# Kernel tuning notes

Measured on AMD Instinct MI355X. Metric: run time of the kernel, lower is better.

Reference implementation:

```python
import jax, jax.numpy as jnp
import numpy as np

D = 512          # d_model
DS = 32          # d_state
EXPAND = 2
HEADDIM = 64
R = 4            # mimo_rank
DIN = EXPAND * D             # 1024 inner dim
H = DIN // HEADDIM           # 16 heads
DFF = ((int(D * 8 / 3) + 7) // 8) * 8  # 1368 SwiGLU hidden
CHUNK = max(1, 64 // R)      # 16
BATCH, SEQ = 4, 512


def setup_inputs() -> dict:
    key = jax.random.key(0)
    ks = jax.random.split(key, 12)
    def w(k, shape, fan):
        return jax.random.normal(k, shape, jnp.float32) / np.float32(np.sqrt(fan))
    return {
        "x": jax.random.normal(ks[0], (BATCH, SEQ, D), jnp.float32),
        "mask": jnp.ones((BATCH, SEQ), jnp.float32),
        "norm1_w": jnp.ones((D,), jnp.float32),
        "norm2_w": jnp.ones((D,), jnp.float32),
        "Wz": w(ks[1], (D, DIN), D),
        "Wx": w(ks[2], (D, DIN), D),
        "Wb": w(ks[3], (D, H * R * DS), D),
        "Wc": w(ks[4], (D, H * R * DS), D),
        "Wdt": w(ks[5], (D, H), D),
        "dt_bias": jnp.zeros((H,), jnp.float32),
        "A_log": jnp.log(jnp.arange(1, H + 1, dtype=jnp.float32)),
        "D_skip": jnp.ones((H,), jnp.float32),
        "Wout": w(ks[6], (DIN, D), DIN),
        "w1": w(ks[7], (D, DFF), D),
        "w2": w(ks[8], (DFF, D), DFF),
        "w3": w(ks[9], (D, DFF), D),
    }


def rmsnorm(x, wgt, eps=1e-6):
    rms = jnp.sqrt(jnp.mean(x * x, axis=-1, keepdims=True) + eps)
    return x / rms * wgt


def ssm_mixer(x, Wz, Wx, Wb, Wc, Wdt, dt_bias, A_log, D_skip, Wout):
    # x: [B, S, D] (already masked)
    B, S, _ = x.shape
    pad = (CHUNK - S % CHUNK) % CHUNK
    if pad > 0:
        x = jnp.pad(x, ((0, 0), (0, pad), (0, 0)))
    Sp = x.shape[1]
    z = x @ Wz                                        # [B,Sp,DIN] gate
    u = (x @ Wx).reshape(B, Sp, H, HEADDIM)           # [B,Sp,H,P]
    Bm = (x @ Wb).reshape(B, Sp, H, R, DS)            # [B,Sp,H,R,N]
    Cm = (x @ Wc).reshape(B, Sp, H, R, DS)
    dt = jax.nn.softplus(x @ Wdt + dt_bias)           # [B,Sp,H]
    a = jnp.exp(dt * (-jnp.exp(A_log)))               # per-step decay [B,Sp,H]
    ud = u * dt[..., None]                            # discretized input

    def step(h, inp):
        a_t, B_t, C_t, ud_t = inp                     # [B,H], [B,H,R,N], [B,H,R,N], [B,H,P]
        h = a_t[:, :, None, None, None] * h + jnp.einsum('bhrn,bhp->bhrnp', B_t, ud_t)
        y = jnp.einsum('bhrn,bhrnp->bhp', C_t, h)
        return h, y

    h0 = jnp.zeros((B, H, R, DS, HEADDIM), x.dtype)
    xs = (a.swapaxes(0, 1), Bm.swapaxes(0, 1), Cm.swapaxes(0, 1), ud.swapaxes(0, 1))
    _, ys = jax.lax.scan(step, h0, xs)                # ys: [Sp,B,H,P]
    y = ys.swapaxes(0, 1) + u * D_skip[None, None, :, None]
    y = y.reshape(B, Sp, DIN) * jax.nn.silu(z)
    y = y @ Wout                                      # [B,Sp,D]
    return y[:, :S]


def reference(x, mask, norm1_w, norm2_w, Wz, Wx, Wb, Wc, Wdt, dt_bias,
              A_log, D_skip, Wout, w1, w2, w3):
    m = mask[..., None]
    xn = rmsnorm(x, norm1_w) * m
    y = ssm_mixer(xn, Wz, Wx, Wb, Wc, Wdt, dt_bias, A_log, D_skip, Wout) * m
    x = x + y
    xn2 = rmsnorm(x, norm2_w)
    x = x + (jax.nn.silu(xn2 @ w1) * (xn2 @ w3)) @ w2
    return x * m
```

## Files before the change

kernel.cpp:

```cpp
#include <hip/hip_runtime.h>
#include <hip/hip_bf16.h>
#include <math.h>

#define Bn 4
#define Sn 512
#define Dn 512
#define DINn 1024
#define Hn 16
#define Pn 64
#define RNn 128
#define DFFn 1368
#define KP2 1408
#define BSn (Bn*Sn)
#define CH 64
#define NCH (Sn/CH)
#define PSTR 6144
#define FSTR 2736
#define FPAD 2816
#define NSCAN (Bn*NCH*Hn)

typedef __attribute__((ext_vector_type(8))) short short8;
typedef __attribute__((ext_vector_type(4))) float f32x4;
typedef __attribute__((ext_vector_type(4))) short short4v;

static __device__ __forceinline__ float bf2f(__hip_bfloat16 v){return __bfloat162float(v);}
static __device__ __forceinline__ __hip_bfloat16 f2bf(float v){return __float2bfloat16(v);}
static __device__ __forceinline__ short f2bfs(float v){ __hip_bfloat16 b=f2bf(v); short s; __builtin_memcpy(&s,&b,2); return s; }
static __device__ __forceinline__ float bfs2f(short s){ __hip_bfloat16 b; __builtin_memcpy(&b,&s,2); return bf2f(b); }

typedef const __attribute__((address_space(1))) unsigned int* gas1_u32p;
typedef __attribute__((address_space(3))) unsigned int* gas3_u32p;
static __device__ __forceinline__ void gl_lds16(const void* g, void* l) {
  __builtin_amdgcn_global_load_lds((gas1_u32p)g, (gas3_u32p)l, 16, 0, 0);
}

struct T8 {
  const float* src[8];
  __hip_bfloat16* dst[8];
  int Rr[8], Cc[8], RrPad[8], CcPad[8], gw[8];
  int start[9];
};

static __device__ __forceinline__ void transpose_tile(const T8& d, int bid, int t,
                                                      float (*tile)[65]) {
  int i = 0;
#pragma unroll
  for (int k = 1; k < 8; ++k) if (bid >= d.start[k]) i = k;
  int rel = bid - d.start[i];
  int gx = rel % d.gw[i], gy = rel / d.gw[i];
  const float* in = d.src[i];
  __hip_bfloat16* out = d.dst[i];
  int Rr = d.Rr[i], Cc = d.Cc[i], RrPad = d.RrPad[i], CcPad = d.CcPad[i];
  int tx = t & 15, ty = t >> 4;
#pragma unroll
  for (int i4 = 0; i4 < 4; ++i4) {
    int r = gy * 64 + ty + i4 * 16;
    int c0 = gx * 64 + tx * 4;
    f32x4 v = (f32x4){0.f, 0.f, 0.f, 0.f};
    if (r < Rr && c0 + 3 < Cc) v = *(const f32x4*)(in + (size_t)r * Cc + c0);
    tile[ty + i4 * 16][tx * 4 + 0] = v[0];
    tile[ty + i4 * 16][tx * 4 + 1] = v[1];
    tile[ty + i4 * 16][tx * 4 + 2] = v[2];
    tile[ty + i4 * 16][tx * 4 + 3] = v[3];
  }
  __syncthreads();
#pragma unroll
  for (int i4 = 0; i4 < 4; ++i4) {
    int r2 = gx * 64 + ty + i4 * 16;
    int c2 = gy * 64 + tx * 4;
    if (r2 < CcPad && c2 + 3 < RrPad) {
      int k = ty + i4 * 16;
      short4v o;
      o.x = f2bfs(tile[tx * 4 + 0][k]);
      o.y = f2bfs(tile[tx * 4 + 1][k]);
      o.z = f2bfs(tile[tx * 4 + 2][k]);
      o.w = f2bfs(tile[tx * 4 + 3][k]);
      *(short4v*)((short*)out + (size_t)r2 * RrPad + c2) = o;
    }
  }
}

__global__ __launch_bounds__(256) void prep_kernel(
    T8 d, const float* __restrict__ x, const float* __restrict__ w,
    const float* __restrict__ mask, const float* __restrict__ Wdt,
    const float* __restrict__ dtb, const float* __restrict__ Alog,
    __hip_bfloat16* __restrict__ outb, float* __restrict__ dt,
    float* __restrict__ la, int tstart) {
  __shared__ float tile[64][65];
  __shared__ float xs[Dn];
  __shared__ float red[4];
  int bid = blockIdx.x, t = threadIdx.x;
  if (bid < tstart) {
    transpose_tile(d, bid, t, tile);
  } else {
    int row = bid - tstart;
    const float* xr = x + (size_t)row * Dn;
    float v0 = xr[t], v1 = xr[t + 256];
    float ss = v0 * v0 + v1 * v1;
#pragma unroll
    for (int o = 32; o > 0; o >>= 1) ss += __shfl_down(ss, o);
    if ((t & 63) == 0) red[t >> 6] = ss;
    __syncthreads();
    float tot = red[0] + red[1] + red[2] + red[3];
    float sc = rsqrtf(tot * (1.f / Dn) + 1e-6f) * mask[row];
    float o0 = v0 * sc * w[t], o1v = v1 * sc * w[t + 256];
    outb[(size_t)row * Dn + t] = f2bf(o0);
    outb[(size_t)row * Dn + t + 256] = f2bf(o1v);
    xs[t] = o0;
    xs[t + 256] = o1v;
    __syncthreads();
    int h = t >> 4, j = t & 15;
    float s = 0.f;
#pragma unroll
    for (int kk = 0; kk < 32; ++kk) {
      int k = j + kk * 16;
      s = fmaf(xs[k], Wdt[k * Hn + h], s);
    }
#pragma unroll
    for (int o = 8; o > 0; o >>= 1) s += __shfl_down(s, o, 16);
    if (j == 0) {
      float v = s + dtb[h];
      float sp = (v > 20.f) ? v : log1pf(expf(v));
      float Ah = expf(Alog[h]);
      dt[(size_t)row * Hn + h] = sp;
      la[(size_t)row * Hn + h] = -Ah * sp;
    }
  }
}

__global__ void rmsnorm2_kernel(const float* __restrict__ x,
                                const float* __restrict__ w,
                                __hip_bfloat16* __restrict__ out) {
  int row = blockIdx.x, t = threadIdx.x;
  const float* xr = x + (size_t)row * Dn;
  float v0 = xr[t], v1 = xr[t + 256];
  float ss = v0 * v0 + v1 * v1;
#pragma unroll
  for (int o = 32; o > 0; o >>= 1) ss += __shfl_down(ss, o);
  __shared__ float red[4];
  if ((t & 63) == 0) red[t >> 6] = ss;
  __syncthreads();
  float tot = red[0] + red[1] + red[2] + red[3];
  float sc = rsqrtf(tot * (1.f / Dn) + 1e-6f);
  out[(size_t)row * Dn + t] = f2bf(v0 * sc * w[t]);
  out[(size_t)row * Dn + t + 256] = f2bf(v1 * sc * w[t + 256]);
}

__global__ __launch_bounds__(256) void gemm_kernel(
    const __hip_bfloat16* __restrict__ A, const __hip_bfloat16* __restrict__ BT,
    __hip_bfloat16* __restrict__ C, int M, int N, int K) {
  __shared__ short As[2][4096];
  __shared__ short Bs[2][4096];
  int m0 = blockIdx.x * 128, n0 = blockIdx.y * 128;
  int t = threadIdx.x;
  int lane = t & 63, wv = t >> 6;
  int wm = (wv & 1) * 64, wn = (wv >> 1) * 64;
  f32x4 acc[4][4];
#pragma unroll
  for (int i = 0; i < 4; ++i)
#pragma unroll
    for (int j = 0; j < 4; ++j) acc[i][j] = (f32x4){0.f, 0.f, 0.f, 0.f};
  const short* Ag = (const short*)A;
  const short* Bg = (const short*)BT;
  int r0 = t >> 2, p = t & 3;
  int q0 = (p - (r0 >> 1)) & 3;
  int r1 = r0 + 64;
  int q1 = (p - (r1 >> 1)) & 3;
  const short* Asrc0 = Ag + (size_t)(m0 + r0) * K + 8 * q0;
  const short* Asrc1 = Ag + (size_t)(m0 + r1) * K + 8 * q1;
  const short* Bsrc0 = Bg + (size_t)(n0 + r0) * K + 8 * q0;
  const short* Bsrc1 = Bg + (size_t)(n0 + r1) * K + 8 * q1;
  int fr = lane & 15, fq = lane >> 4;
  int kTiles = K >> 5;
  auto stage = [&](int buf, int k0) {
    gl_lds16(Asrc0 + k0, &As[buf][wv * 512]);
    gl_lds16(Asrc1 + k0, &As[buf][2048 + wv * 512]);
    gl_lds16(Bsrc0 + k0, &Bs[buf][wv * 512]);
    gl_lds16(Bsrc1 + k0, &Bs[buf][2048 + wv * 512]);
  };
  auto domfma = [&](int buf) {
    short8 af[4], bfr[4];
#pragma unroll
    for (int i = 0; i < 4; ++i) {
      int rr = wm + i * 16 + fr;
      af[i] = *(const short8*)&As[buf][rr * 32 + (((rr >> 1) + fq) & 3) * 8];
    }
#pragma unroll
    for (int i = 0; i < 4; ++i) {
      int rr = wn + i * 16 + fr;
      bfr[i] = *(const short8*)&Bs[buf][rr * 32 + (((rr >> 1) + fq) & 3) * 8];
    }
#pragma unroll
    for (int mi = 0; mi < 4; ++mi)
#pragma unroll
      for (int ni = 0; ni < 4; ++ni)
        acc[mi][ni] = __builtin_amdgcn_mfma_f32_16x16x32_bf16(af[mi], bfr[ni], acc[mi][ni], 0, 0, 0);
  };
  stage(0, 0);
  for (int kt = 0; kt < kTiles; ++kt) {
    int buf = kt & 1;
    __syncthreads();
    if (kt + 1 < kTiles) stage(buf ^ 1, (kt + 1) << 5);
    domfma(buf);
  }
  int fq4 = (lane >> 4) * 4;
#pragma unroll
  for (int mi = 0; mi < 4; ++mi)
#pragma unroll
    for (int ni = 0; ni < 4; ++ni) {
      int col = n0 + wn + ni * 16 + fr;
      if (col < N) {
        int rowb = m0 + wm + mi * 16 + fq4;
#pragma unroll
        for (int r = 0; r < 4; ++r)
          C[(size_t)(rowb + r) * N + col] = f2bf(acc[mi][ni][r]);
      }
    }
}

template <int MODE>
__global__ __launch_bounds__(256) void gemm64_ep_kernel(
    const __hip_bfloat16* __restrict__ A, const __hip_bfloat16* __restrict__ BT,
    const float* __restrict__ aux, const float* __restrict__ mask,
    float* __restrict__ out, int M, int N, int K) {
  __shared__ short As[2][64][72];
  __shared__ short Bs[2][64][72];
  int m0 = blockIdx.x * 64, n0 = blockIdx.y * 64;
  int t = threadIdx.x;
  int lane = t & 63, wv = t >> 6;
  int wm = (wv & 1) * 32, wn = (wv >> 1) * 32;
  f32x4 acc[2][2];
#pragma unroll
  for (int i = 0; i < 2; ++i)
#pragma unroll
    for (int j = 0; j < 2; ++j) acc[i][j] = (f32x4){0.f, 0.f, 0.f, 0.f};
  const short* Ag = (const short*)A;
  const short* Bg = (const short*)BT;
  int sr = t >> 2;
  int sc = (t & 3) * 16;
  const short* Ap = Ag + (size_t)(m0 + sr) * K + sc;
  const short* Bp = Bg + (size_t)(n0 + sr) * K + sc;
  int fr = lane & 15, fq = (lane >> 4) * 8;
  int kTiles = K >> 6;
  short8 a0A = 0, a1A = 0, b0A = 0, b1A = 0;
  short8 a0B = 0, a1B = 0, b0B = 0, b1B = 0;
  auto loadA = [&](int k0) {
    a0A = *(const short8*)(Ap + k0);
    a1A = *(const short8*)(Ap + k0 + 8);
    b0A = *(const short8*)(Bp + k0);
    b1A = *(const short8*)(Bp + k0 + 8);
  };
  auto loadB = [&](int k0) {
    a0B = *(const short8*)(Ap + k0);
    a1B = *(const short8*)(Ap + k0 + 8);
    b0B = *(const short8*)(Bp + k0);
    b1B = *(const short8*)(Bp + k0 + 8);
  };
  auto storeA = [&](int buf) {
    *(short8*)&As[buf][sr][sc] = a0A;
    *(short8*)&As[buf][sr][sc + 8] = a1A;
    *(short8*)&Bs[buf][sr][sc] = b0A;
    *(short8*)&Bs[buf][sr][sc + 8] = b1A;
  };
  auto storeB = [&](int buf) {
    *(short8*)&As[buf][sr][sc] = a0B;
    *(short8*)&As[buf][sr][sc + 8] = a1B;
    *(short8*)&Bs[buf][sr][sc] = b0B;
    *(short8*)&Bs[buf][sr][sc + 8] = b1B;
  };
  auto mfma = [&](int buf) {
#pragma unroll
    for (int kk = 0; kk < 2; ++kk) {
      short8 af[2], bfr[2];
#pragma unroll
      for (int i = 0; i < 2; ++i) af[i] = *(const short8*)&As[buf][wm + i * 16 + fr][kk * 32 + fq];
#pragma unroll
      for (int i = 0; i < 2; ++i) bfr[i] = *(const short8*)&Bs[buf][wn + i * 16 + fr][kk * 32 + fq];
#pragma unroll
      for (int mi = 0; mi < 2; ++mi)
#pragma unroll
        for (int ni = 0; ni < 2; ++ni)
          acc[mi][ni] = __builtin_amdgcn_mfma_f32_16x16x32_bf16(af[mi], bfr[ni], acc[mi][ni], 0, 0, 0);
    }
  };
  loadA(0);
  storeA(0);
  loadA(64);
  __syncthreads();
  for (int kt = 0; kt < kTiles; kt += 2) {
    storeA(1);
    if (kt + 2 < kTiles) loadB((kt + 2) << 6);
    mfma(0);
    __syncthreads();
    if (kt + 2 < kTiles) storeB(0);
    if (kt + 3 < kTiles) loadA((kt + 3) << 6);
    mfma(1);
    __syncthreads();
  }
  int fq4 = (lane >> 4) * 4;
#pragma unroll
  for (int mi = 0; mi < 2; ++mi)
#pragma unroll
    for (int ni = 0; ni < 2; ++ni) {
      int col = n0 + wn + ni * 16 + fr;
#pragma unroll
      for (int r = 0; r < 4; ++r) {
        int row = m0 + wm + mi * 16 + fq4 + r;
        float m = mask[row];
        size_t a = (size_t)row * N + col;
        float v = acc[mi][ni][r];
        if (MODE == 1) out[a] = aux[a] + v * m;
        else           out[a] = (aux[a] + v) * m;
      }
    }
}

__global__ __launch_bounds__(256) void gemm64g_kernel(
    const __hip_bfloat16* __restrict__ A, const __hip_bfloat16* __restrict__ BT,
    __hip_bfloat16* __restrict__ G, int M, int K) {
  __shared__ short As[2][64][72];
  __shared__ short B1s[2][64][72];
  __shared__ short B3s[2][64][72];
  int m0 = blockIdx.x * 64, n0 = blockIdx.y * 64;
  int t = threadIdx.x;
  int lane = t & 63, wv = t >> 6;
  int wm = (wv & 1) * 32, wn = (wv >> 1) * 32;
  f32x4 acc1[2][2], acc3[2][2];
#pragma unroll
  for (int i = 0; i < 2; ++i)
#pragma unroll
    for (int j = 0; j < 2; ++j) {
      acc1[i][j] = (f32x4){0.f, 0.f, 0.f, 0.f};
      acc3[i][j] = (f32x4){0.f, 0.f, 0.f, 0.f};
    }
  const short* Ag = (const short*)A;
  const short* Bg = (const short*)BT;
  int sr = t >> 2;
  int sc = (t & 3) * 16;
  const short* Ap  = Ag + (size_t)(m0 + sr) * K + sc;
  const short* B1p = Bg + (size_t)(n0 + sr) * K + sc;
  const short* B3p = Bg + (size_t)(DFFn + n0 + sr) * K + sc;
  int fr = lane & 15, fq = (lane >> 4) * 8;
  int kTiles = K >> 6;
  short8 a0A = 0, a1A = 0, c0A = 0, c1A = 0, d0A = 0, d1A = 0;
  short8 a0B = 0, a1B = 0, c0B = 0, c1B = 0, d0B = 0, d1B = 0;
  auto loadA = [&](int k0) {
    a0A = *(const short8*)(Ap + k0);
    a1A = *(const short8*)(Ap + k0 + 8);
    c0A = *(const short8*)(B1p + k0);
    c1A = *(const short8*)(B1p + k0 + 8);
    d0A = *(const short8*)(B3p + k0);
    d1A = *(const short8*)(B3p + k0 + 8);
  };
  auto loadB = [&](int k0) {
    a0B = *(const short8*)(Ap + k0);
    a1B = *(const short8*)(Ap + k0 + 8);
    c0B = *(const short8*)(B1p + k0);
    c1B = *(const short8*)(B1p + k0 + 8);
    d0B = *(const short8*)(B3p + k0);
    d1B = *(const short8*)(B3p + k0 + 8);
  };
  auto storeA = [&](int buf) {
    *(short8*)&As[buf][sr][sc] = a0A;
    *(short8*)&As[buf][sr][sc + 8] = a1A;
    *(short8*)&B1s[buf][sr][sc] = c0A;
    *(short8*)&B1s[buf][sr][sc + 8] = c1A;
    *(short8*)&B3s[buf][sr][sc] = d0A;
    *(short8*)&B3s[buf][sr][sc + 8] = d1A;
  };
  auto storeB = [&](int buf) {
    *(short8*)&As[buf][sr][sc] = a0B;
    *(short8*)&As[buf][sr][sc + 8] = a1B;
    *(short8*)&B1s[buf][sr][sc] = c0B;
    *(short8*)&B1s[buf][sr][sc + 8] = c1B;
    *(short8*)&B3s[buf][sr][sc] = d0B;
    *(short8*)&B3s[buf][sr][sc + 8] = d1B;
  };
  auto mfma = [&](int buf) {
#pragma unroll
    for (int kk = 0; kk < 2; ++kk) {
      short8 af[2], b1f[2], b3f[2];
#pragma unroll
      for (int i = 0; i < 2; ++i) af[i]  = *(const short8*)&As[buf][wm + i * 16 + fr][kk * 32 + fq];
#pragma unroll
      for (int i = 0; i < 2; ++i) b1f[i] = *(const short8*)&B1s[buf][wn + i * 16 + fr][kk * 32 + fq];
#pragma unroll
      for (int i = 0; i < 2; ++i) b3f[i] = *(const short8*)&B3s[buf][wn + i * 16 + fr][kk * 32 + fq];
#pragma unroll
      for (int mi = 0; mi < 2; ++mi)
#pragma unroll
        for (int ni = 0; ni < 2; ++ni) {
          acc1[mi][ni] = __builtin_amdgcn_mfma_f32_16x16x32_bf16(af[mi], b1f[ni], acc1[mi][ni], 0, 0, 0);
          acc3[mi][ni] = __builtin_amdgcn_mfma_f32_16x16x32_bf16(af[mi], b3f[ni], acc3[mi][ni], 0, 0, 0);
        }
    }
  };
  loadA(0);
  storeA(0);
  loadA(64);
  __syncthreads();
  for (int kt = 0; kt < kTiles; kt += 2) {
    storeA(1);
    if (kt + 2 < kTiles) loadB((kt + 2) << 6);
    mfma(0);
    __syncthreads();
    if (kt + 2 < kTiles) storeB(0);
    if (kt + 3 < kTiles) loadA((kt + 3) << 6);
    mfma(1);
    __syncthreads();
  }
  int fq4 = (lane >> 4) * 4;
#pragma unroll
  for (int mi = 0; mi < 2; ++mi)
#pragma unroll
    for (int ni = 0; ni < 2; ++ni) {
      int col = n0 + wn + ni * 16 + fr;
      bool valid = col < DFFn;
#pragma unroll
      for (int r = 0; r < 4; ++r) {
        int row = m0 + wm + mi * 16 + fq4 + r;
        float h1v = acc1[mi][ni][r];
        float sil = h1v / (1.f + __expf(-h1v));
        float g = sil * acc3[mi][ni][r];
        G[(size_t)row * KP2 + col] = valid ? f2bf(g) : f2bf(0.f);
      }
    }
}

__global__ __launch_bounds__(256) void chunk_intra_kernel(
    T8 d, int nscan, const __hip_bfloat16* __restrict__ P, const float* __restrict__ dt,
    const float* __restrict__ la, __hip_bfloat16* __restrict__ ysb,
    __hip_bfloat16* __restrict__ Sbuf, float* __restrict__ ecL, float* __restrict__ ec) {
  __shared__ __align__(16) char smem[55040];
  int bid0 = blockIdx.x;
  int t = threadIdx.x;
  if (bid0 >= nscan) {
    transpose_tile(d, bid0 - nscan, t, (float(*)[65])smem);
    return;
  }
  int id = bid0;
  int h = id & 15, c = (id >> 4) & 7, b = id >> 7;
  int lane = t & 63, wv = t >> 6;
  short* sCB = (short*)smem;
  short* sB  = (short*)(smem + 18432);
  short* sUD = (short*)(smem + 35840);
  short* sG  = (short*)(smem + 45056);
  float* scum = (float*)(smem + 54272);
  float* sws  = scum + 64;
  float* sdt  = sws + 64;
  int row0 = b * Sn + c * CH;
  const short* Pb = (const short*)P;
#pragma unroll
  for (int i = 0; i < 4; ++i) {
    int idx = t + i * 256;
    int r = idx >> 4, kk = (idx & 15) * 8;
    *(short8*)&sCB[r * 136 + kk] = *(const short8*)(Pb + (size_t)(row0 + r) * PSTR + 4096 + h * 128 + kk);
    *(short8*)&sB [r * 136 + kk] = *(const short8*)(Pb + (size_t)(row0 + r) * PSTR + 2048 + h * 128 + kk);
  }
  if (t < 64) { sdt[t] = dt[(size_t)(row0 + t) * Hn + h]; scum[t] = la[(size_t)(row0 + t) * Hn + h]; }
  __syncthreads();
  if (wv == 0) {
    float v = scum[lane];
#pragma unroll
    for (int o = 1; o < 64; o <<= 1) { float n = __shfl_up(v, o); if (lane >= o) v += n; }
    scum[lane] = v;
    float c63 = __shfl(v, 63);
    sws[lane] = __expf(c63 - v);
    ec[((size_t)((b * NCH + c) * Hn + h)) * 64 + lane] = __expf(v);
    if (lane == 0) ecL[(b * NCH + c) * Hn + h] = __expf(c63);
  }
#pragma unroll
  for (int i = 0; i < 2; ++i) {
    int idx = t + i * 256;
    int s = idx >> 3, pc = (idx & 7) * 8;
    short8 uv = *(const short8*)(Pb + (size_t)(row0 + s) * PSTR + 1024 + h * 64 + pc);
    float dv = sdt[s];
#pragma unroll
    for (int j = 0; j < 8; ++j) sUD[(pc + j) * 72 + s] = f2bfs(bfs2f(uv[j]) * dv);
  }
  __syncthreads();
  int fr = lane & 15, fq = (lane >> 4) * 8, q4 = (lane >> 4) * 4;
  {
    short8 af[4];
#pragma unroll
    for (int k = 0; k < 4; ++k) af[k] = *(short8*)&sCB[(16 * wv + fr) * 136 + k * 32 + fq];
#pragma unroll
    for (int j = 0; j < 4; ++j) {
      f32x4 acc = (f32x4){0.f, 0.f, 0.f, 0.f};
#pragma unroll
      for (int k = 0; k < 4; ++k) {
        short8 bf = *(short8*)&sB[(16 * j + fr) * 136 + k * 32 + fq];
        acc = __builtin_amdgcn_mfma_f32_16x16x32_bf16(af[k], bf, acc, 0, 0, 0);
      }
      int ss = 16 * j + fr;
      float cs = scum[ss];
#pragma unroll
      for (int r = 0; r < 4; ++r) {
        int tt = 16 * wv + q4 + r;
        float w = (ss <= tt) ? __expf(scum[tt] - cs) : 0.f;
        sG[tt * 72 + ss] = f2bfs(acc[r] * w);
      }
    }
  }
  __syncthreads();
#pragma unroll
  for (int i = 0; i < 32; ++i) {
    int idx = t + i * 256;
    int rn = idx >> 6, s = idx & 63;
    sCB[rn * 72 + s] = f2bfs(bfs2f(sB[s * 136 + rn]) * sws[s]);
  }
  __syncthreads();
  {
    short8 ag[2];
#pragma unroll
    for (int k = 0; k < 2; ++k) ag[k] = *(short8*)&sG[(16 * wv + fr) * 72 + k * 32 + fq];
#pragma unroll
    for (int j = 0; j < 4; ++j) {
      f32x4 acc = (f32x4){0.f, 0.f, 0.f, 0.f};
#pragma unroll
      for (int k = 0; k < 2; ++k) {
        short8 bf = *(short8*)&sUD[(16 * j + fr) * 72 + k * 32 + fq];
        acc = __builtin_amdgcn_mfma_f32_16x16x32_bf16(ag[k], bf, acc, 0, 0, 0);
      }
#pragma unroll
      for (int r = 0; r < 4; ++r)
        ysb[(size_t)(row0 + 16 * wv + q4 + r) * DINn + h * 64 + 16 * j + fr] = f2bf(acc[r]);
    }
  }
#pragma unroll
  for (int mt0 = 0; mt0 < 2; ++mt0) {
    int mt = wv * 2 + mt0;
    short8 ab[2];
#pragma unroll
    for (int k = 0; k < 2; ++k) ab[k] = *(short8*)&sCB[(16 * mt + fr) * 72 + k * 32 + fq];
#pragma unroll
    for (int j = 0; j < 4; ++j) {
      f32x4 acc = (f32x4){0.f, 0.f, 0.f, 0.f};
#pragma unroll
      for (int k = 0; k < 2; ++k) {
        short8 bf = *(short8*)&sUD[(16 * j + fr) * 72 + k * 32 + fq];
        acc = __builtin_amdgcn_mfma_f32_16x16x32_bf16(ab[k], bf, acc, 0, 0, 0);
      }
#pragma unroll
      for (int r = 0; r < 4; ++r)
        ((short*)Sbuf)[((size_t)((b * NCH + c) * Hn + h) * RNn + 16 * mt + q4 + r) * 64 + 16 * j + fr] =
            f2bfs(acc[r]);
    }
  }
}

__global__ void chunk_state_kernel(const __hip_bfloat16* __restrict__ Sbuf,
                                   const float* __restrict__ ecL,
                                   __hip_bfloat16* __restrict__ Hp) {
  int bh = blockIdx.x >> 4;
  int j = ((blockIdx.x & 15) * 256 + threadIdx.x) * 2;
  int b = bh >> 4, h = bh & 15;
  const short* Sb = (const short*)Sbuf;
  short* Hs = (short*)Hp;
  float hp0 = 0.f, hp1 = 0.f;
#pragma unroll
  for (int c = 0; c < NCH; ++c) {
    size_t addr = ((size_t)((b * NCH + c) * Hn + h)) * 8192 + j;
    short2 sv = *(const short2*)(Sb + addr);
    *(short2*)(Hs + addr) = make_short2(f2bfs(hp0), f2bfs(hp1));
    float e = ecL[(b * NCH + c) * Hn + h];
    hp0 = e * hp0 + bfs2f(sv.x);
    hp1 = e * hp1 + bfs2f(sv.y);
  }
}

__global__ __launch_bounds__(256) void inter_gate_kernel(
    const __hip_bfloat16* __restrict__ P, const __hip_bfloat16* __restrict__ Hp,
    const float* __restrict__ ec, const __hip_bfloat16* __restrict__ ysb,
    const float* __restrict__ Dsk, __hip_bfloat16* __restrict__ y2b) {
  int id = blockIdx.x;
  int h = id & 15, c = (id >> 4) & 7, b = id >> 7;
  int t = threadIdx.x, lane = t & 63, wv = t >> 6;
  __shared__ __align__(16) short sC[64 * 136];
  __shared__ __align__(16) short sHt[64 * 136];
  __shared__ __align__(16) short sz[64 * 64];
  __shared__ __align__(16) short su[64 * 64];
  __shared__ float sec[64];
  int row0 = b * Sn + c * CH;
  const short* Pb = (const short*)P;
#pragma unroll
  for (int i = 0; i < 2; ++i) {
    int idx = t + i * 256;
    int r = idx >> 3, pc = (idx & 7) * 8;
    *(short8*)&sz[r * 64 + pc] = *(const short8*)(Pb + (size_t)(row0 + r) * PSTR + h * 64 + pc);
    *(short8*)&su[r * 64 + pc] = *(const short8*)(Pb + (size_t)(row0 + r) * PSTR + 1024 + h * 64 + pc);
  }
  if (c > 0) {
    const short* Hps = (const short*)Hp;
    size_t hbase = ((size_t)((b * NCH + c) * Hn + h)) * 8192;
#pragma unroll
    for (int i = 0; i < 4; ++i) {
      int idx = t + i * 256;
      int r = idx >> 4, kk = (idx & 15) * 8;
      *(short8*)&sC[r * 136 + kk] = *(const short8*)(Pb + (size_t)(row0 + r) * PSTR + 4096 + h * 128 + kk);
    }
#pragma unroll
    for (int i = 0; i < 32; ++i) {
      int idx = t + i * 256;
      int rn = idx >> 6, p = idx & 63;
      sHt[p * 136 + rn] = Hps[hbase + idx];
    }
    if (t < 64) sec[t] = ec[((size_t)((b * NCH + c) * Hn + h)) * 64 + t];
  }
  __syncthreads();
  int fr = lane & 15, fq = (lane >> 4) * 8, q4 = (lane >> 4) * 4;
  f32x4 acc[4];
#pragma unroll
  for (int j = 0; j < 4; ++j) acc[j] = (f32x4){0.f, 0.f, 0.f, 0.f};
  if (c > 0) {
    short8 af[4];
#pragma unroll
    for (int k = 0; k < 4; ++k) af[k] = *(short8*)&sC[(16 * wv + fr) * 136 + k * 32 + fq];
#pragma unroll
    for (int j = 0; j < 4; ++j)
#pragma unroll
      for (int k = 0; k < 4; ++k) {
        short8 bf = *(short8*)&sHt[(16 * j + fr) * 136 + k * 32 + fq];
        acc[j] = __builtin_amdgcn_mfma_f32_16x16x32_bf16(af[k], bf, acc[j], 0, 0, 0);
      }
  }
  float dsk = Dsk[h];
#pragma unroll
  for (int j = 0; j < 4; ++j) {
    int col = 16 * j + fr;
#pragma unroll
    for (int r = 0; r < 4; ++r) {
      int tt = 16 * wv + q4 + r;
      size_t a = (size_t)(row0 + tt) * DINn + h * 64 + col;
      float val = bf2f(ysb[a]);
      if (c > 0) val += sec[tt] * acc[j][r];
      float uu = bfs2f(su[tt * 64 + col]);
      float zz = bfs2f(sz[tt * 64 + col]);
      float sil = zz / (1.f + __expf(-zz));
      y2b[a] = f2bf((val + uu * dsk) * sil);
    }
  }
}

extern "C" void kernel_launch(void* const* d_in, const int* in_sizes, int n_in,
                              void* d_out, int out_size, void* d_ws, size_t ws_size,
                              hipStream_t stream) {
  const float* x    = (const float*)d_in[0];
  const float* mask = (const float*)d_in[1];
  const float* n1w  = (const float*)d_in[2];
  const float* n2w  = (const float*)d_in[3];
  const float* Wz   = (const float*)d_in[4];
  const float* Wx   = (const float*)d_in[5];
  const float* Wb   = (const float*)d_in[6];
  const float* Wc   = (const float*)d_in[7];
  const float* Wdt  = (const float*)d_in[8];
  const float* dtb  = (const float*)d_in[9];
  const float* Alog = (const float*)d_in[10];
  const float* Dsk  = (const float*)d_in[11];
  const float* Wout = (const float*)d_in[12];
  const float* w1   = (const float*)d_in[13];
  const float* w2   = (const float*)d_in[14];
  const float* w3   = (const float*)d_in[15];

  char* ws = (char*)d_ws;
  size_t off = 0;
  auto alloc = [&](size_t bytes) {
    char* p = ws + off;
    off += (bytes + 255) & ~(size_t)255;
    return p;
  };
  __hip_bfloat16* xnb = (__hip_bfloat16*)alloc((size_t)BSn * Dn * 2);
  __hip_bfloat16* P = (__hip_bfloat16*)alloc((size_t)BSn * PSTR * 2);
  float* dt  = (float*)alloc((size_t)BSn * Hn * 4);
  float* la  = (float*)alloc((size_t)BSn * Hn * 4);
  __hip_bfloat16* ysb = (__hip_bfloat16*)alloc((size_t)BSn * DINn * 2);
  float* ecL = (float*)alloc((size_t)Bn * NCH * Hn * 4);
  float* ec  = (float*)alloc((size_t)Bn * NCH * Hn * 64 * 4);
  __hip_bfloat16* WallT = (__hip_bfloat16*)alloc((size_t)PSTR * Dn * 2);
  __hip_bfloat16* WoutT = (__hip_bfloat16*)alloc((size_t)Dn * DINn * 2);
  __hip_bfloat16* w13T  = (__hip_bfloat16*)alloc((size_t)FPAD * Dn * 2);
  __hip_bfloat16* w2T   = (__hip_bfloat16*)alloc((size_t)Dn * KP2 * 2);
  char* arena = alloc(22000000);
  __hip_bfloat16* Sbuf = (__hip_bfloat16*)arena;
  __hip_bfloat16* Hp   = (__hip_bfloat16*)(arena + 8388608);
  __hip_bfloat16* y2b  = (__hip_bfloat16*)(arena + 16777216);
  float* xres          = (float*)arena;
  __hip_bfloat16* gatedb = (__hip_bfloat16*)(arena + 4194304);

  auto buildT8 = [](T8& td, int n) {
    int tot = 0;
    for (int i = 0; i < n; ++i) {
      td.gw[i] = (td.CcPad[i] + 63) / 64;
      int gh = (td.RrPad[i] + 63) / 64;
      td.start[i] = tot;
      tot += td.gw[i] * gh;
    }
    for (int i = n; i < 9; ++i) td.start[i] = tot;
    return tot;
  };
  T8 tdE;
  tdE.src[0] = Wz; tdE.dst[0] = WallT;                      tdE.Rr[0] = 512; tdE.Cc[0] = 1024; tdE.RrPad[0] = 512; tdE.CcPad[0] = 1024;
  tdE.src[1] = Wx; tdE.dst[1] = WallT + (size_t)1024 * 512; tdE.Rr[1] = 512; tdE.Cc[1] = 1024; tdE.RrPad[1] = 512; tdE.CcPad[1] = 1024;
  tdE.src[2] = Wb; tdE.dst[2] = WallT + (size_t)2048 * 512; tdE.Rr[2] = 512; tdE.Cc[2] = 2048; tdE.RrPad[2] = 512; tdE.CcPad[2] = 2048;
  tdE.src[3] = Wc; tdE.dst[3] = WallT + (size_t)4096 * 512; tdE.Rr[3] = 512; tdE.Cc[3] = 2048; tdE.RrPad[3] = 512; tdE.CcPad[3] = 2048;
  int totE = buildT8(tdE, 4);
  T8 tdL;
  tdL.src[0] = Wout; tdL.dst[0] = WoutT;                     tdL.Rr[0] = 1024; tdL.Cc[0] = 512;  tdL.RrPad[0] = 1024; tdL.CcPad[0] = 512;
  tdL.src[1] = w1;   tdL.dst[1] = w13T;                      tdL.Rr[1] = 512;  tdL.Cc[1] = 1368; tdL.RrPad[1] = 512;  tdL.CcPad[1] = 1368;
  tdL.src[2] = w3;   tdL.dst[2] = w13T + (size_t)1368 * 512; tdL.Rr[2] = 512;  tdL.Cc[2] = 1368; tdL.RrPad[2] = 512;  tdL.CcPad[2] = 1448;
  tdL.src[3] = w2;   tdL.dst[3] = w2T;                       tdL.Rr[3] = 1368; tdL.Cc[3] = 512;  tdL.RrPad[3] = KP2;  tdL.CcPad[3] = 512;
  int totL = buildT8(tdL, 4);

  prep_kernel<<<totE + BSn, 256, 0, stream>>>(tdE, x, n1w, mask, Wdt, dtb, Alog, xnb, dt, la, totE);
  gemm_kernel<<<dim3(16, 48), 256, 0, stream>>>(xnb, WallT, P, BSn, PSTR, Dn);
  chunk_intra_kernel<<<NSCAN + totL, 256, 0, stream>>>(tdL, NSCAN, P, dt, la, ysb, Sbuf, ecL, ec);
  chunk_state_kernel<<<Bn * Hn * 16, 256, 0, stream>>>(Sbuf, ecL, Hp);
  inter_gate_kernel<<<Bn * NCH * Hn, 256, 0, stream>>>(P, Hp, ec, ysb, Dsk, y2b);
  gemm64_ep_kernel<1><<<dim3(32, 8), 256, 0, stream>>>(y2b, WoutT, x, mask, xres, BSn, Dn, DINn);
  rmsnorm2_kernel<<<BSn, 256, 0, stream>>>(xres, n2w, xnb);
  gemm64g_kernel<<<dim3(32, KP2 / 64), 256, 0, stream>>>(xnb, w13T, gatedb, BSn, Dn);
  gemm64_ep_kernel<2><<<dim3(32, 8), 256, 0, stream>>>(gatedb, w2T, xres, mask, (float*)d_out, BSn, Dn, KP2);
}
```

Measured before the change: 210.3 us.

## Fuse inter-chunk state recurrence into gate kernel and RMSNorm2 into FFN GEMM

Removes the separate chunk_state kernel: each inter_gate block now rebuilds its incoming state by summing the earlier chunk states, weighted by products of chunk decays, read straight from Sbuf, whose layout is transposed to suit this. The second RMSNorm kernel goes away: the Wout GEMM epilogue atomically adds per-row sums of squares, and the FFN GEMM applies the normalisation while converting fp32 activations to bf16 on load. All weight transposes move into prep_kernel, which also zeroes the row-sum buffer. Together this saves two launches and the Hp round trip through memory. In exchange, later chunks repeat O(c) state reads, atomics are added, and the FFN A-operand is read as fp32.

```diff
diff --git a/kernel.cpp b/kernel.cpp
--- a/kernel.cpp
+++ b/kernel.cpp
@@ -15,7 +15,6 @@
 #define CH 64
 #define NCH (Sn/CH)
 #define PSTR 6144
-#define FSTR 2736
 #define FPAD 2816
 #define NSCAN (Bn*NCH*Hn)
 
@@ -85,14 +84,14 @@
     const float* __restrict__ mask, const float* __restrict__ Wdt,
     const float* __restrict__ dtb, const float* __restrict__ Alog,
     __hip_bfloat16* __restrict__ outb, float* __restrict__ dt,
-    float* __restrict__ la, int tstart) {
+    float* __restrict__ la, float* __restrict__ rs, int tstart) {
   __shared__ float tile[64][65];
   __shared__ float xs[Dn];
   __shared__ float red[4];
   int bid = blockIdx.x, t = threadIdx.x;
   if (bid < tstart) {
     transpose_tile(d, bid, t, tile);
-  } else {
+  } else if (bid - tstart < BSn) {
     int row = bid - tstart;
     const float* xr = x + (size_t)row * Dn;
     float v0 = xr[t], v1 = xr[t + 256];
@@ -125,25 +124,10 @@
       dt[(size_t)row * Hn + h] = sp;
       la[(size_t)row * Hn + h] = -Ah * sp;
     }
-  }
-}
-
-__global__ void rmsnorm2_kernel(const float* __restrict__ x,
-                                const float* __restrict__ w,
-                                __hip_bfloat16* __restrict__ out) {
-  int row = blockIdx.x, t = threadIdx.x;
-  const float* xr = x + (size_t)row * Dn;
-  float v0 = xr[t], v1 = xr[t + 256];
-  float ss = v0 * v0 + v1 * v1;
-#pragma unroll
-  for (int o = 32; o > 0; o >>= 1) ss += __shfl_down(ss, o);
-  __shared__ float red[4];
-  if ((t & 63) == 0) red[t >> 6] = ss;
-  __syncthreads();
-  float tot = red[0] + red[1] + red[2] + red[3];
-  float sc = rsqrtf(tot * (1.f / Dn) + 1e-6f);
-  out[(size_t)row * Dn + t] = f2bf(v0 * sc * w[t]);
-  out[(size_t)row * Dn + t + 256] = f2bf(v1 * sc * w[t + 256]);
+  } else {
+    *(f32x4*)&rs[t * 8]     = (f32x4){0.f, 0.f, 0.f, 0.f};
+    *(f32x4*)&rs[t * 8 + 4] = (f32x4){0.f, 0.f, 0.f, 0.f};
+  }
 }
 
 __global__ __launch_bounds__(256) void gemm_kernel(
@@ -222,7 +206,7 @@
 __global__ __launch_bounds__(256) void gemm64_ep_kernel(
     const __hip_bfloat16* __restrict__ A, const __hip_bfloat16* __restrict__ BT,
     const float* __restrict__ aux, const float* __restrict__ mask,
-    float* __restrict__ out, int M, int N, int K) {
+    float* __restrict__ out, float* __restrict__ rs, int M, int N, int K) {
   __shared__ short As[2][64][72];
   __shared__ short Bs[2][64][72];
   int m0 = blockIdx.x * 64, n0 = blockIdx.y * 64;
@@ -298,6 +282,11 @@
     __syncthreads();
   }
   int fq4 = (lane >> 4) * 4;
+  float rsum[2][4];
+#pragma unroll
+  for (int mi = 0; mi < 2; ++mi)
+#pragma unroll
+    for (int r = 0; r < 4; ++r) rsum[mi][r] = 0.f;
 #pragma unroll
   for (int mi = 0; mi < 2; ++mi)
 #pragma unroll
@@ -309,18 +298,40 @@
         float m = mask[row];
         size_t a = (size_t)row * N + col;
         float v = acc[mi][ni][r];
-        if (MODE == 1) out[a] = aux[a] + v * m;
-        else           out[a] = (aux[a] + v) * m;
-      }
-    }
+        if (MODE == 1) {
+          float ov = aux[a] + v * m;
+          out[a] = ov;
+          rsum[mi][r] += ov * ov;
+        } else {
+          out[a] = (aux[a] + v) * m;
+        }
+      }
+    }
+  if (MODE == 1) {
+#pragma unroll
+    for (int mi = 0; mi < 2; ++mi)
+#pragma unroll
+      for (int r = 0; r < 4; ++r) {
+        float s = rsum[mi][r];
+#pragma unroll
+        for (int o = 8; o > 0; o >>= 1) s += __shfl_xor(s, o);
+        if ((lane & 15) == 0) {
+          int row = m0 + wm + mi * 16 + fq4 + r;
+          atomicAdd(&rs[row], s);
+        }
+      }
+  }
 }
 
 __global__ __launch_bounds__(256) void gemm64g_kernel(
-    const __hip_bfloat16* __restrict__ A, const __hip_bfloat16* __restrict__ BT,
+    const float* __restrict__ X, const float* __restrict__ rs,
+    const float* __restrict__ n2w, const __hip_bfloat16* __restrict__ BT,
     __hip_bfloat16* __restrict__ G, int M, int K) {
   __shared__ short As[2][64][72];
   __shared__ short B1s[2][64][72];
   __shared__ short B3s[2][64][72];
+  __shared__ float ssc[64];
+  __shared__ float sw[Dn];
   int m0 = blockIdx.x * 64, n0 = blockIdx.y * 64;
   int t = threadIdx.x;
   int lane = t & 63, wv = t >> 6;
@@ -333,28 +344,43 @@
       acc1[i][j] = (f32x4){0.f, 0.f, 0.f, 0.f};
       acc3[i][j] = (f32x4){0.f, 0.f, 0.f, 0.f};
     }
-  const short* Ag = (const short*)A;
   const short* Bg = (const short*)BT;
   int sr = t >> 2;
   int sc = (t & 3) * 16;
-  const short* Ap  = Ag + (size_t)(m0 + sr) * K + sc;
+  const float* Xp  = X + (size_t)(m0 + sr) * Dn + sc;
   const short* B1p = Bg + (size_t)(n0 + sr) * K + sc;
   const short* B3p = Bg + (size_t)(DFFn + n0 + sr) * K + sc;
   int fr = lane & 15, fq = (lane >> 4) * 8;
   int kTiles = K >> 6;
+  if (t < 64) ssc[t] = rsqrtf(rs[m0 + t] * (1.f / Dn) + 1e-6f);
+  sw[t] = n2w[t];
+  sw[t + 256] = n2w[t + 256];
+  __syncthreads();
+  float scl = ssc[sr];
   short8 a0A = 0, a1A = 0, c0A = 0, c1A = 0, d0A = 0, d1A = 0;
   short8 a0B = 0, a1B = 0, c0B = 0, c1B = 0, d0B = 0, d1B = 0;
+  auto cvtA = [&](int k0, short8& lo, short8& hi) {
+    f32x4 v[4];
+#pragma unroll
+    for (int q = 0; q < 4; ++q) v[q] = *(const f32x4*)(Xp + k0 + q * 4);
+    short tmp[16];
+#pragma unroll
+    for (int q = 0; q < 4; ++q)
+#pragma unroll
+      for (int jj = 0; jj < 4; ++jj)
+        tmp[q * 4 + jj] = f2bfs(v[q][jj] * scl * sw[k0 + sc + q * 4 + jj]);
+    __builtin_memcpy(&lo, tmp, 16);
+    __builtin_memcpy(&hi, tmp + 8, 16);
+  };
   auto loadA = [&](int k0) {
-    a0A = *(const short8*)(Ap + k0);
-    a1A = *(const short8*)(Ap + k0 + 8);
+    cvtA(k0, a0A, a1A);
     c0A = *(const short8*)(B1p + k0);
     c1A = *(const short8*)(B1p + k0 + 8);
     d0A = *(const short8*)(B3p + k0);
     d1A = *(const short8*)(B3p + k0 + 8);
   };
   auto loadB = [&](int k0) {
-    a0B = *(const short8*)(Ap + k0);
-    a1B = *(const short8*)(Ap + k0 + 8);
+    cvtA(k0, a0B, a1B);
     c0B = *(const short8*)(B1p + k0);
     c1B = *(const short8*)(B1p + k0 + 8);
     d0B = *(const short8*)(B3p + k0);
@@ -428,19 +454,13 @@
 }
 
 __global__ __launch_bounds__(256) void chunk_intra_kernel(
-    T8 d, int nscan, const __hip_bfloat16* __restrict__ P, const float* __restrict__ dt,
+    const __hip_bfloat16* __restrict__ P, const float* __restrict__ dt,
     const float* __restrict__ la, __hip_bfloat16* __restrict__ ysb,
     __hip_bfloat16* __restrict__ Sbuf, float* __restrict__ ecL, float* __restrict__ ec) {
+  int id = blockIdx.x;
+  int h = id & 15, c = (id >> 4) & 7, b = id >> 7;
+  int t = threadIdx.x, lane = t & 63, wv = t >> 6;
   __shared__ __align__(16) char smem[55040];
-  int bid0 = blockIdx.x;
-  int t = threadIdx.x;
-  if (bid0 >= nscan) {
-    transpose_tile(d, bid0 - nscan, t, (float(*)[65])smem);
-    return;
-  }
-  int id = bid0;
-  int h = id & 15, c = (id >> 4) & 7, b = id >> 7;
-  int lane = t & 63, wv = t >> 6;
   short* sCB = (short*)smem;
   short* sB  = (short*)(smem + 18432);
   short* sUD = (short*)(smem + 35840);
@@ -541,38 +561,20 @@
         short8 bf = *(short8*)&sUD[(16 * j + fr) * 72 + k * 32 + fq];
         acc = __builtin_amdgcn_mfma_f32_16x16x32_bf16(ab[k], bf, acc, 0, 0, 0);
       }
-#pragma unroll
-      for (int r = 0; r < 4; ++r)
-        ((short*)Sbuf)[((size_t)((b * NCH + c) * Hn + h) * RNn + 16 * mt + q4 + r) * 64 + 16 * j + fr] =
-            f2bfs(acc[r]);
-    }
-  }
-}
-
-__global__ void chunk_state_kernel(const __hip_bfloat16* __restrict__ Sbuf,
-                                   const float* __restrict__ ecL,
-                                   __hip_bfloat16* __restrict__ Hp) {
-  int bh = blockIdx.x >> 4;
-  int j = ((blockIdx.x & 15) * 256 + threadIdx.x) * 2;
-  int b = bh >> 4, h = bh & 15;
-  const short* Sb = (const short*)Sbuf;
-  short* Hs = (short*)Hp;
-  float hp0 = 0.f, hp1 = 0.f;
-#pragma unroll
-  for (int c = 0; c < NCH; ++c) {
-    size_t addr = ((size_t)((b * NCH + c) * Hn + h)) * 8192 + j;
-    short2 sv = *(const short2*)(Sb + addr);
-    *(short2*)(Hs + addr) = make_short2(f2bfs(hp0), f2bfs(hp1));
-    float e = ecL[(b * NCH + c) * Hn + h];
-    hp0 = e * hp0 + bfs2f(sv.x);
-    hp1 = e * hp1 + bfs2f(sv.y);
+      int pp = 16 * j + fr;
+      int rn0 = 16 * mt + q4;
+      short4v o;
+      o.x = f2bfs(acc[0]); o.y = f2bfs(acc[1]); o.z = f2bfs(acc[2]); o.w = f2bfs(acc[3]);
+      *(short4v*)&((short*)Sbuf)[((size_t)((b * NCH + c) * Hn + h) * 64 + pp) * 128 + rn0] = o;
+    }
   }
 }
 
 __global__ __launch_bounds__(256) void inter_gate_kernel(
-    const __hip_bfloat16* __restrict__ P, const __hip_bfloat16* __restrict__ Hp,
-    const float* __restrict__ ec, const __hip_bfloat16* __restrict__ ysb,
-    const float* __restrict__ Dsk, __hip_bfloat16* __restrict__ y2b) {
+    const __hip_bfloat16* __restrict__ P, const __hip_bfloat16* __restrict__ Sbuf,
+    const float* __restrict__ ecL, const float* __restrict__ ec,
+    const __hip_bfloat16* __restrict__ ysb, const float* __restrict__ Dsk,
+    __hip_bfloat16* __restrict__ y2b) {
   int id = blockIdx.x;
   int h = id & 15, c = (id >> 4) & 7, b = id >> 7;
   int t = threadIdx.x, lane = t & 63, wv = t >> 6;
@@ -591,19 +593,42 @@
     *(short8*)&su[r * 64 + pc] = *(const short8*)(Pb + (size_t)(row0 + r) * PSTR + 1024 + h * 64 + pc);
   }
   if (c > 0) {
-    const short* Hps = (const short*)Hp;
-    size_t hbase = ((size_t)((b * NCH + c) * Hn + h)) * 8192;
 #pragma unroll
     for (int i = 0; i < 4; ++i) {
       int idx = t + i * 256;
       int r = idx >> 4, kk = (idx & 15) * 8;
       *(short8*)&sC[r * 136 + kk] = *(const short8*)(Pb + (size_t)(row0 + r) * PSTR + 4096 + h * 128 + kk);
     }
-#pragma unroll
-    for (int i = 0; i < 32; ++i) {
-      int idx = t + i * 256;
-      int rn = idx >> 6, p = idx & 63;
-      sHt[p * 136 + rn] = Hps[hbase + idx];
+    float wch[8];
+    {
+      float w = 1.f;
+      for (int cp = c - 1; cp >= 0; --cp) {
+        wch[cp] = w;
+        if (cp > 0) w *= ecL[(size_t)((b * NCH + cp) * Hn + h)];
+      }
+    }
+    float hacc[32];
+#pragma unroll
+    for (int jj = 0; jj < 32; ++jj) hacc[jj] = 0.f;
+    const short* Sb = (const short*)Sbuf;
+    for (int cp = 0; cp < c; ++cp) {
+      size_t base = ((size_t)((b * NCH + cp) * Hn + h)) * 8192 + (size_t)t * 32;
+      float wv2 = wch[cp];
+#pragma unroll
+      for (int v4 = 0; v4 < 4; ++v4) {
+        short8 sv = *(const short8*)(Sb + base + v4 * 8);
+#pragma unroll
+        for (int jj = 0; jj < 8; ++jj)
+          hacc[v4 * 8 + jj] = fmaf(wv2, bfs2f(sv[jj]), hacc[v4 * 8 + jj]);
+      }
+    }
+    int p = t >> 2, rn0 = (t & 3) * 32;
+#pragma unroll
+    for (int v4 = 0; v4 < 4; ++v4) {
+      short8 o;
+#pragma unroll
+      for (int jj = 0; jj < 8; ++jj) o[jj] = f2bfs(hacc[v4 * 8 + jj]);
+      *(short8*)&sHt[p * 136 + rn0 + v4 * 8] = o;
     }
     if (t < 64) sec[t] = ec[((size_t)((b * NCH + c) * Hn + h)) * 64 + t];
   }
@@ -676,48 +701,40 @@
   __hip_bfloat16* ysb = (__hip_bfloat16*)alloc((size_t)BSn * DINn * 2);
   float* ecL = (float*)alloc((size_t)Bn * NCH * Hn * 4);
   float* ec  = (float*)alloc((size_t)Bn * NCH * Hn * 64 * 4);
+  float* rs  = (float*)alloc((size_t)BSn * 4);
   __hip_bfloat16* WallT = (__hip_bfloat16*)alloc((size_t)PSTR * Dn * 2);
   __hip_bfloat16* WoutT = (__hip_bfloat16*)alloc((size_t)Dn * DINn * 2);
   __hip_bfloat16* w13T  = (__hip_bfloat16*)alloc((size_t)FPAD * Dn * 2);
   __hip_bfloat16* w2T   = (__hip_bfloat16*)alloc((size_t)Dn * KP2 * 2);
   char* arena = alloc(22000000);
   __hip_bfloat16* Sbuf = (__hip_bfloat16*)arena;
-  __hip_bfloat16* Hp   = (__hip_bfloat16*)(arena + 8388608);
   __hip_bfloat16* y2b  = (__hip_bfloat16*)(arena + 16777216);
   float* xres          = (float*)arena;
   __hip_bfloat16* gatedb = (__hip_bfloat16*)(arena + 4194304);
 
-  auto buildT8 = [](T8& td, int n) {
-    int tot = 0;
-    for (int i = 0; i < n; ++i) {
-      td.gw[i] = (td.CcPad[i] + 63) / 64;
-      int gh = (td.RrPad[i] + 63) / 64;
-      td.start[i] = tot;
-      tot += td.gw[i] * gh;
-    }
-    for (int i = n; i < 9; ++i) td.start[i] = tot;
-    return tot;
-  };
-  T8 tdE;
-  tdE.src[0] = Wz; tdE.dst[0] = WallT;                      tdE.Rr[0] = 512; tdE.Cc[0] = 1024; tdE.RrPad[0] = 512; tdE.CcPad[0] = 1024;
-  tdE.src[1] = Wx; tdE.dst[1] = WallT + (size_t)1024 * 512; tdE.Rr[1] = 512; tdE.Cc[1] = 1024; tdE.RrPad[1] = 512; tdE.CcPad[1] = 1024;
-  tdE.src[2] = Wb; tdE.dst[2] = WallT + (size_t)2048 * 512; tdE.Rr[2] = 512; tdE.Cc[2] = 2048; tdE.RrPad[2] = 512; tdE.CcPad[2] = 2048;
-  tdE.src[3] = Wc; tdE.dst[3] = WallT + (size_t)4096 * 512; tdE.Rr[3] = 512; tdE.Cc[3] = 2048; tdE.RrPad[3] = 512; tdE.CcPad[3] = 2048;
-  int totE = buildT8(tdE, 4);
-  T8 tdL;
-  tdL.src[0] = Wout; tdL.dst[0] = WoutT;                     tdL.Rr[0] = 1024; tdL.Cc[0] = 512;  tdL.RrPad[0] = 1024; tdL.CcPad[0] = 512;
-  tdL.src[1] = w1;   tdL.dst[1] = w13T;                      tdL.Rr[1] = 512;  tdL.Cc[1] = 1368; tdL.RrPad[1] = 512;  tdL.CcPad[1] = 1368;
-  tdL.src[2] = w3;   tdL.dst[2] = w13T + (size_t)1368 * 512; tdL.Rr[2] = 512;  tdL.Cc[2] = 1368; tdL.RrPad[2] = 512;  tdL.CcPad[2] = 1448;
-  tdL.src[3] = w2;   tdL.dst[3] = w2T;                       tdL.Rr[3] = 1368; tdL.Cc[3] = 512;  tdL.RrPad[3] = KP2;  tdL.CcPad[3] = 512;
-  int totL = buildT8(tdL, 4);
-
-  prep_kernel<<<totE + BSn, 256, 0, stream>>>(tdE, x, n1w, mask, Wdt, dtb, Alog, xnb, dt, la, totE);
+  T8 td;
+  td.src[0] = Wz;   td.dst[0] = WallT;                      td.Rr[0] = 512;  td.Cc[0] = 1024; td.RrPad[0] = 512;  td.CcPad[0] = 1024;
+  td.src[1] = Wx;   td.dst[1] = WallT + (size_t)1024 * 512; td.Rr[1] = 512;  td.Cc[1] = 1024; td.RrPad[1] = 512;  td.CcPad[1] = 1024;
+  td.src[2] = Wb;   td.dst[2] = WallT + (size_t)2048 * 512; td.Rr[2] = 512;  td.Cc[2] = 2048; td.RrPad[2] = 512;  td.CcPad[2] = 2048;
+  td.src[3] = Wc;   td.dst[3] = WallT + (size_t)4096 * 512; td.Rr[3] = 512;  td.Cc[3] = 2048; td.RrPad[3] = 512;  td.CcPad[3] = 2048;
+  td.src[4] = Wout; td.dst[4] = WoutT;                      td.Rr[4] = 1024; td.Cc[4] = 512;  td.RrPad[4] = 1024; td.CcPad[4] = 512;
+  td.src[5] = w1;   td.dst[5] = w13T;                       td.Rr[5] = 512;  td.Cc[5] = 1368; td.RrPad[5] = 512;  td.CcPad[5] = 1368;
+  td.src[6] = w3;   td.dst[6] = w13T + (size_t)1368 * 512;  td.Rr[6] = 512;  td.Cc[6] = 1368; td.RrPad[6] = 512;  td.CcPad[6] = 1448;
+  td.src[7] = w2;   td.dst[7] = w2T;                        td.Rr[7] = 1368; td.Cc[7] = 512;  td.RrPad[7] = KP2;  td.CcPad[7] = 512;
+  int tot = 0;
+  for (int i = 0; i < 8; ++i) {
+    td.gw[i] = (td.CcPad[i] + 63) / 64;
+    int gh = (td.RrPad[i] + 63) / 64;
+    td.start[i] = tot;
+    tot += td.gw[i] * gh;
+  }
+  td.start[8] = tot;
+
+  prep_kernel<<<tot + BSn + 1, 256, 0, stream>>>(td, x, n1w, mask, Wdt, dtb, Alog, xnb, dt, la, rs, tot);
   gemm_kernel<<<dim3(16, 48), 256, 0, stream>>>(xnb, WallT, P, BSn, PSTR, Dn);
-  chunk_intra_kernel<<<NSCAN + totL, 256, 0, stream>>>(tdL, NSCAN, P, dt, la, ysb, Sbuf, ecL, ec);
-  chunk_state_kernel<<<Bn * Hn * 16, 256, 0, stream>>>(Sbuf, ecL, Hp);
-  inter_gate_kernel<<<Bn * NCH * Hn, 256, 0, stream>>>(P, Hp, ec, ysb, Dsk, y2b);
-  gemm64_ep_kernel<1><<<dim3(32, 8), 256, 0, stream>>>(y2b, WoutT, x, mask, xres, BSn, Dn, DINn);
-  rmsnorm2_kernel<<<BSn, 256, 0, stream>>>(xres, n2w, xnb);
-  gemm64g_kernel<<<dim3(32, KP2 / 64), 256, 0, stream>>>(xnb, w13T, gatedb, BSn, Dn);
-  gemm64_ep_kernel<2><<<dim3(32, 8), 256, 0, stream>>>(gatedb, w2T, xres, mask, (float*)d_out, BSn, Dn, KP2);
-}
+  chunk_intra_kernel<<<NSCAN, 256, 0, stream>>>(P, dt, la, ysb, Sbuf, ecL, ec);
+  inter_gate_kernel<<<NSCAN, 256, 0, stream>>>(P, Sbuf, ecL, ec, ysb, Dsk, y2b);
+  gemm64_ep_kernel<1><<<dim3(32, 8), 256, 0, stream>>>(y2b, WoutT, x, mask, xres, rs, BSn, Dn, DINn);
+  gemm64g_kernel<<<dim3(32, KP2 / 64), 256, 0, stream>>>(xres, rs, n2w, w13T, gatedb, BSn, Dn);
+  gemm64_ep_kernel<2><<<dim3(32, 8), 256, 0, stream>>>(gatedb, w2T, xres, mask, (float*)d_out, rs, BSn, Dn, KP2);
+}
```

Measured after the change: 212.6 us. No clear change (+1.1%).
